# Performance work log

Measured on AMD Instinct MI355X. Metric: run time of the kernel, lower is better.

## Reference

```python
import jax, jax.numpy as jnp
import numpy as np

B, H, D, N = 4, 16, 64, 2048

def setup_inputs() -> dict:
    key = jax.random.key(0)
    kq, kk, kv = jax.random.split(key, 3)
    q = jax.random.normal(kq, (B, H, D, N), dtype=jnp.float32)
    k = jax.random.normal(kk, (B, H, D, N), dtype=jnp.float32)
    v = jax.random.normal(kv, (B, H, D, N), dtype=jnp.float32)
    return {"q": q, "k": k, "v": v}

def reference(q, k, v):
    # layout: (b, h, d, n); scale uses head_dim = q.shape[-2]
    scale = q.shape[-2] ** (-0.5)
    sim = jnp.einsum('bhdi,bhdj->bhij', q * scale, k)  # [B,H,N,N]
    attn = jax.nn.softmax(sim, axis=-1)  # stable softmax (internally subtracts max)
    out = jnp.einsum('bhij,bhdj->bhdi', attn, v)  # [B,H,D,N]
    return out
```

## Files before the change

### kernel.cpp

```cpp
#include <hip/hip_runtime.h>


#define DDIM 64
#define NSEQ 2048
#define STR  72
#define ROWB (STR * 2)
#define BUFB (128 * ROWB)

typedef _Float16 half8   __attribute__((ext_vector_type(8)));
typedef _Float16 half4v  __attribute__((ext_vector_type(4)));
typedef _Float16 half2v  __attribute__((ext_vector_type(2)));
typedef float    float4v __attribute__((ext_vector_type(4)));

__global__ __launch_bounds__(256, 2) void attn_fwd(
    const float* __restrict__ qg, const float* __restrict__ kg,
    const float* __restrict__ vg, float* __restrict__ og) {
  __shared__ __align__(16) char smem[2 * BUFB];

  const int t    = threadIdx.x;
  const int lane = t & 63;
  const int w    = t >> 6;
  const int n16  = lane & 15;
  const int quad = lane >> 4;

  const int bid  = blockIdx.x;
  const int head = ((bid & 7) << 3) | (bid >> 6);
  const int tile = (bid >> 3) & 7;
  const int i0   = tile * 256;

  const float* qh = qg + (size_t)head * DDIM * NSEQ;
  const float* kh = kg + (size_t)head * DDIM * NSEQ;
  const float* vh = vg + (size_t)head * DDIM * NSEQ;

  const int dp  = t & 31;
  const int iqq = t >> 5;
  const int vd  = t >> 2;
  const int qq  = t & 3;

  const float* kp = kh + (2 * dp) * NSEQ;
  const float* vp = vh + vd * NSEQ;

  float4v ka0, kb0, ka1, kb1, va0, vb0, va1, vb1;
  ka0 = *(const float4v*)(kp + iqq * 4);
  kb0 = *(const float4v*)(kp + NSEQ + iqq * 4);
  ka1 = *(const float4v*)(kp + (iqq + 8) * 4);
  kb1 = *(const float4v*)(kp + NSEQ + (iqq + 8) * 4);
  va0 = *(const float4v*)(vp + qq * 4);
  vb0 = *(const float4v*)(vp + qq * 4 + 16);
  va1 = *(const float4v*)(vp + 32 + qq * 4);
  vb1 = *(const float4v*)(vp + 48 + qq * 4);

  {
    _Float16* Qt = (_Float16*)smem;
    const float mul = 0.125f * 1.44269504088896340736f;
#pragma unroll
    for (int h = 0; h < 8; ++h) {
      const float* r0 = qh + (2 * dp) * NSEQ + i0 + h * 32 + iqq * 4;
      float4v a = *(const float4v*)(r0);
      float4v b = *(const float4v*)(r0 + NSEQ);
      _Float16* base = Qt + (h * 32 + iqq * 4) * STR + 2 * dp;
#pragma unroll
      for (int s = 0; s < 4; ++s) {
        half2v hh = {(_Float16)(a[s] * mul), (_Float16)(b[s] * mul)};
        *(half2v*)(base + s * STR) = hh;
      }
    }
  }
  __syncthreads();

  const _Float16* Qt = (const _Float16*)smem;
  half8 bq[4][2];
#pragma unroll
  for (int ig = 0; ig < 4; ++ig) {
    bq[ig][0] = *(const half8*)(Qt + (w * 64 + ig * 16 + n16) * STR + quad * 8);
    bq[ig][1] = *(const half8*)(Qt + (w * 64 + ig * 16 + n16) * STR + 32 + quad * 8);
  }
  __syncthreads();

  const half8 ones = {1.0f16, 1.0f16, 1.0f16, 1.0f16,
                      1.0f16, 1.0f16, 1.0f16, 1.0f16};

  float4v o[4][4];
  float4v lac[4];
#pragma unroll
  for (int ig = 0; ig < 4; ++ig) {
#pragma unroll
    for (int dt = 0; dt < 4; ++dt) o[ig][dt] = (float4v){0.f, 0.f, 0.f, 0.f};
    lac[ig] = (float4v){0.f, 0.f, 0.f, 0.f};
  }

  {
    _Float16* Ktw = (_Float16*)(smem + BUFB);
    _Float16* baseA = Ktw + (iqq * 4) * STR + 2 * dp;
    _Float16* baseB = Ktw + ((iqq + 8) * 4) * STR + 2 * dp;
#pragma unroll
    for (int s = 0; s < 4; ++s) {
      half2v ha = {(_Float16)ka0[s], (_Float16)kb0[s]};
      *(half2v*)(baseA + s * STR) = ha;
      half2v hb = {(_Float16)ka1[s], (_Float16)kb1[s]};
      *(half2v*)(baseB + s * STR) = hb;
    }
    _Float16* Vw = Ktw + 64 * STR + vd * STR;
    half8 h0 = {(_Float16)va0[0], (_Float16)va0[1], (_Float16)va0[2], (_Float16)va0[3],
                (_Float16)vb0[0], (_Float16)vb0[1], (_Float16)vb0[2], (_Float16)vb0[3]};
    *(half8*)(Vw + qq * 8) = h0;
    half8 h1 = {(_Float16)va1[0], (_Float16)va1[1], (_Float16)va1[2], (_Float16)va1[3],
                (_Float16)vb1[0], (_Float16)vb1[1], (_Float16)vb1[2], (_Float16)vb1[3]};
    *(half8*)(Vw + (qq + 4) * 8) = h1;
  }
  __syncthreads();

  for (int kt = 0; kt < 32; ++kt) {
    const _Float16* Kt = (const _Float16*)(smem + ((kt + 1) & 1) * BUFB);
    const _Float16* Vt = Kt + 64 * STR;

    if (kt < 31) {
      const int j1 = (kt + 1) * 64;
      ka0 = *(const float4v*)(kp + j1 + iqq * 4);
      kb0 = *(const float4v*)(kp + NSEQ + j1 + iqq * 4);
      ka1 = *(const float4v*)(kp + j1 + (iqq + 8) * 4);
      kb1 = *(const float4v*)(kp + NSEQ + j1 + (iqq + 8) * 4);
      va0 = *(const float4v*)(vp + j1 + qq * 4);
      vb0 = *(const float4v*)(vp + j1 + qq * 4 + 16);
      va1 = *(const float4v*)(vp + j1 + 32 + qq * 4);
      vb1 = *(const float4v*)(vp + j1 + 48 + qq * 4);
    }

    half4v p[4][4];
#pragma unroll
    for (int jt = 0; jt < 4; ++jt) {
      half8 kfa = *(const half8*)(Kt + (jt * 16 + n16) * STR + quad * 8);
      half8 kfb = *(const half8*)(Kt + (jt * 16 + n16) * STR + 32 + quad * 8);
#pragma unroll
      for (int ig = 0; ig < 4; ++ig) {
        float4v sa = {0.f, 0.f, 0.f, 0.f};
        sa = __builtin_amdgcn_mfma_f32_16x16x32_f16(kfa, bq[ig][0], sa, 0, 0, 0);
        sa = __builtin_amdgcn_mfma_f32_16x16x32_f16(kfb, bq[ig][1], sa, 0, 0, 0);
        p[ig][jt] = (half4v){(_Float16)__builtin_amdgcn_exp2f(sa[0]),
                             (_Float16)__builtin_amdgcn_exp2f(sa[1]),
                             (_Float16)__builtin_amdgcn_exp2f(sa[2]),
                             (_Float16)__builtin_amdgcn_exp2f(sa[3])};
      }
    }

    half8 pg[4][2];
#pragma unroll
    for (int ig = 0; ig < 4; ++ig) {
      pg[ig][0] = __builtin_shufflevector(p[ig][0], p[ig][1], 0, 1, 2, 3, 4, 5, 6, 7);
      pg[ig][1] = __builtin_shufflevector(p[ig][2], p[ig][3], 0, 1, 2, 3, 4, 5, 6, 7);
    }

#pragma unroll
    for (int ig = 0; ig < 4; ++ig) {
      lac[ig] = __builtin_amdgcn_mfma_f32_16x16x32_f16(ones, pg[ig][0], lac[ig], 0, 0, 0);
      lac[ig] = __builtin_amdgcn_mfma_f32_16x16x32_f16(ones, pg[ig][1], lac[ig], 0, 0, 0);
    }

#pragma unroll
    for (int dt = 0; dt < 4; ++dt) {
#pragma unroll
      for (int g = 0; g < 2; ++g) {
        half8 va = *(const half8*)(Vt + (dt * 16 + n16) * STR + (g * 4 + quad) * 8);
#pragma unroll
        for (int ig = 0; ig < 4; ++ig) {
          o[ig][dt] = __builtin_amdgcn_mfma_f32_16x16x32_f16(
              va, pg[ig][g], o[ig][dt], 0, 0, 0);
        }
      }
    }

    if (kt < 31) {
      _Float16* Ktw = (_Float16*)(smem + (kt & 1) * BUFB);
      _Float16* baseA = Ktw + (iqq * 4) * STR + 2 * dp;
      _Float16* baseB = Ktw + ((iqq + 8) * 4) * STR + 2 * dp;
#pragma unroll
      for (int s = 0; s < 4; ++s) {
        half2v ha = {(_Float16)ka0[s], (_Float16)kb0[s]};
        *(half2v*)(baseA + s * STR) = ha;
        half2v hb = {(_Float16)ka1[s], (_Float16)kb1[s]};
        *(half2v*)(baseB + s * STR) = hb;
      }
      _Float16* Vw = Ktw + 64 * STR + vd * STR;
      half8 h0 = {(_Float16)va0[0], (_Float16)va0[1], (_Float16)va0[2], (_Float16)va0[3],
                  (_Float16)vb0[0], (_Float16)vb0[1], (_Float16)vb0[2], (_Float16)vb0[3]};
      *(half8*)(Vw + qq * 8) = h0;
      half8 h1 = {(_Float16)va1[0], (_Float16)va1[1], (_Float16)va1[2], (_Float16)va1[3],
                  (_Float16)vb1[0], (_Float16)vb1[1], (_Float16)vb1[2], (_Float16)vb1[3]};
      *(half8*)(Vw + (qq + 4) * 8) = h1;
      __syncthreads();
    }
  }

#pragma unroll
  for (int ig = 0; ig < 4; ++ig) {
    const float inv = 1.0f / lac[ig][0];
    float* ob = og + (size_t)head * DDIM * NSEQ + i0 + w * 64 + ig * 16 + n16;
#pragma unroll
    for (int dt = 0; dt < 4; ++dt) {
#pragma unroll
      for (int r = 0; r < 4; ++r) {
        ob[(size_t)(dt * 16 + quad * 4 + r) * NSEQ] = o[ig][dt][r] * inv;
      }
    }
  }
}

extern "C" void kernel_launch(void* const* d_in, const int* in_sizes, int n_in,
                              void* d_out, int out_size, void* d_ws, size_t ws_size,
                              hipStream_t stream) {
  (void)in_sizes; (void)n_in; (void)d_ws; (void)ws_size; (void)out_size;
  const float* q = (const float*)d_in[0];
  const float* k = (const float*)d_in[1];
  const float* v = (const float*)d_in[2];
  attn_fwd<<<dim3(512), dim3(256), 0, stream>>>(q, k, v, (float*)d_out);
}
```

Baseline: 187.1 us.

## Use 512-thread blocks with 32 query rows per wave and MFMA priority boost

Doubles the block to 8 waves, each handling 32 query rows instead of 64, so every K/V tile staged in shared memory is consumed by more waves. The global loads and fp16 staging of K/V are redistributed over twice as many threads, which halves per-thread load registers and accumulators. It also wraps the PV and row-sum MFMA section in s_setprio so waves issuing matrix work get priority over waves loading. The trade-off is less register-level reuse of each K/V fragment per wave, more LDS fragment reads per MFMA, and heavier barrier cost across 8 waves.

```diff
diff --git a/kernel.cpp b/kernel.cpp
--- a/kernel.cpp
+++ b/kernel.cpp
@@ -12,7 +12,7 @@
 typedef _Float16 half2v  __attribute__((ext_vector_type(2)));
 typedef float    float4v __attribute__((ext_vector_type(4)));
 
-__global__ __launch_bounds__(256, 2) void attn_fwd(
+__global__ __launch_bounds__(512, 4) void attn_fwd(
     const float* __restrict__ qg, const float* __restrict__ kg,
     const float* __restrict__ vg, float* __restrict__ og) {
   __shared__ __align__(16) char smem[2 * BUFB];
@@ -32,33 +32,31 @@
   const float* kh = kg + (size_t)head * DDIM * NSEQ;
   const float* vh = vg + (size_t)head * DDIM * NSEQ;
 
-  const int dp  = t & 31;
-  const int iqq = t >> 5;
-  const int vd  = t >> 2;
-  const int qq  = t & 3;
+  const int dp = t & 31;
+  const int iq = t >> 5;
+  const int vd = t >> 3;
+  const int sj = t & 7;
+  const int vg_ = sj >> 2;
+  const int vq  = sj & 3;
 
-  const float* kp = kh + (2 * dp) * NSEQ;
-  const float* vp = vh + vd * NSEQ;
+  const float* kp  = kh + (2 * dp) * NSEQ + iq * 4;
+  const float* vpA = vh + vd * NSEQ + vg_ * 32 + vq * 4;
 
-  float4v ka0, kb0, ka1, kb1, va0, vb0, va1, vb1;
-  ka0 = *(const float4v*)(kp + iqq * 4);
-  kb0 = *(const float4v*)(kp + NSEQ + iqq * 4);
-  ka1 = *(const float4v*)(kp + (iqq + 8) * 4);
-  kb1 = *(const float4v*)(kp + NSEQ + (iqq + 8) * 4);
-  va0 = *(const float4v*)(vp + qq * 4);
-  vb0 = *(const float4v*)(vp + qq * 4 + 16);
-  va1 = *(const float4v*)(vp + 32 + qq * 4);
-  vb1 = *(const float4v*)(vp + 48 + qq * 4);
+  float4v ka, kb, va, vb;
+  ka = *(const float4v*)(kp);
+  kb = *(const float4v*)(kp + NSEQ);
+  va = *(const float4v*)(vpA);
+  vb = *(const float4v*)(vpA + 16);
 
   {
     _Float16* Qt = (_Float16*)smem;
     const float mul = 0.125f * 1.44269504088896340736f;
 #pragma unroll
-    for (int h = 0; h < 8; ++h) {
-      const float* r0 = qh + (2 * dp) * NSEQ + i0 + h * 32 + iqq * 4;
+    for (int h = 0; h < 4; ++h) {
+      const float* r0 = qh + (2 * dp) * NSEQ + i0 + h * 64 + iq * 4;
       float4v a = *(const float4v*)(r0);
       float4v b = *(const float4v*)(r0 + NSEQ);
-      _Float16* base = Qt + (h * 32 + iqq * 4) * STR + 2 * dp;
+      _Float16* base = Qt + (h * 64 + iq * 4) * STR + 2 * dp;
 #pragma unroll
       for (int s = 0; s < 4; ++s) {
         half2v hh = {(_Float16)(a[s] * mul), (_Float16)(b[s] * mul)};
@@ -69,21 +67,21 @@
   __syncthreads();
 
   const _Float16* Qt = (const _Float16*)smem;
-  half8 bq[4][2];
+  half8 bq[2][2];
 #pragma unroll
-  for (int ig = 0; ig < 4; ++ig) {
-    bq[ig][0] = *(const half8*)(Qt + (w * 64 + ig * 16 + n16) * STR + quad * 8);
-    bq[ig][1] = *(const half8*)(Qt + (w * 64 + ig * 16 + n16) * STR + 32 + quad * 8);
+  for (int ig = 0; ig < 2; ++ig) {
+    bq[ig][0] = *(const half8*)(Qt + (w * 32 + ig * 16 + n16) * STR + quad * 8);
+    bq[ig][1] = *(const half8*)(Qt + (w * 32 + ig * 16 + n16) * STR + 32 + quad * 8);
   }
   __syncthreads();
 
   const half8 ones = {1.0f16, 1.0f16, 1.0f16, 1.0f16,
                       1.0f16, 1.0f16, 1.0f16, 1.0f16};
 
-  float4v o[4][4];
-  float4v lac[4];
+  float4v o[2][4];
+  float4v lac[2];
 #pragma unroll
-  for (int ig = 0; ig < 4; ++ig) {
+  for (int ig = 0; ig < 2; ++ig) {
 #pragma unroll
     for (int dt = 0; dt < 4; ++dt) o[ig][dt] = (float4v){0.f, 0.f, 0.f, 0.f};
     lac[ig] = (float4v){0.f, 0.f, 0.f, 0.f};
@@ -91,22 +89,15 @@
 
   {
     _Float16* Ktw = (_Float16*)(smem + BUFB);
-    _Float16* baseA = Ktw + (iqq * 4) * STR + 2 * dp;
-    _Float16* baseB = Ktw + ((iqq + 8) * 4) * STR + 2 * dp;
+    _Float16* base = Ktw + (iq * 4) * STR + 2 * dp;
 #pragma unroll
     for (int s = 0; s < 4; ++s) {
-      half2v ha = {(_Float16)ka0[s], (_Float16)kb0[s]};
-      *(half2v*)(baseA + s * STR) = ha;
-      half2v hb = {(_Float16)ka1[s], (_Float16)kb1[s]};
-      *(half2v*)(baseB + s * STR) = hb;
+      half2v hh = {(_Float16)ka[s], (_Float16)kb[s]};
+      *(half2v*)(base + s * STR) = hh;
     }
-    _Float16* Vw = Ktw + 64 * STR + vd * STR;
-    half8 h0 = {(_Float16)va0[0], (_Float16)va0[1], (_Float16)va0[2], (_Float16)va0[3],
-                (_Float16)vb0[0], (_Float16)vb0[1], (_Float16)vb0[2], (_Float16)vb0[3]};
-    *(half8*)(Vw + qq * 8) = h0;
-    half8 h1 = {(_Float16)va1[0], (_Float16)va1[1], (_Float16)va1[2], (_Float16)va1[3],
-                (_Float16)vb1[0], (_Float16)vb1[1], (_Float16)vb1[2], (_Float16)vb1[3]};
-    *(half8*)(Vw + (qq + 4) * 8) = h1;
+    half8 hv = {(_Float16)va[0], (_Float16)va[1], (_Float16)va[2], (_Float16)va[3],
+                (_Float16)vb[0], (_Float16)vb[1], (_Float16)vb[2], (_Float16)vb[3]};
+    *(half8*)(Ktw + 64 * STR + vd * STR + sj * 8) = hv;
   }
   __syncthreads();
 
@@ -116,23 +107,19 @@
 
     if (kt < 31) {
       const int j1 = (kt + 1) * 64;
-      ka0 = *(const float4v*)(kp + j1 + iqq * 4);
-      kb0 = *(const float4v*)(kp + NSEQ + j1 + iqq * 4);
-      ka1 = *(const float4v*)(kp + j1 + (iqq + 8) * 4);
-      kb1 = *(const float4v*)(kp + NSEQ + j1 + (iqq + 8) * 4);
-      va0 = *(const float4v*)(vp + j1 + qq * 4);
-      vb0 = *(const float4v*)(vp + j1 + qq * 4 + 16);
-      va1 = *(const float4v*)(vp + j1 + 32 + qq * 4);
-      vb1 = *(const float4v*)(vp + j1 + 48 + qq * 4);
+      ka = *(const float4v*)(kp + j1);
+      kb = *(const float4v*)(kp + NSEQ + j1);
+      va = *(const float4v*)(vpA + j1);
+      vb = *(const float4v*)(vpA + j1 + 16);
     }
 
-    half4v p[4][4];
+    half4v p[2][4];
 #pragma unroll
     for (int jt = 0; jt < 4; ++jt) {
       half8 kfa = *(const half8*)(Kt + (jt * 16 + n16) * STR + quad * 8);
       half8 kfb = *(const half8*)(Kt + (jt * 16 + n16) * STR + 32 + quad * 8);
 #pragma unroll
-      for (int ig = 0; ig < 4; ++ig) {
+      for (int ig = 0; ig < 2; ++ig) {
         float4v sa = {0.f, 0.f, 0.f, 0.f};
         sa = __builtin_amdgcn_mfma_f32_16x16x32_f16(kfa, bq[ig][0], sa, 0, 0, 0);
         sa = __builtin_amdgcn_mfma_f32_16x16x32_f16(kfb, bq[ig][1], sa, 0, 0, 0);
@@ -143,58 +130,52 @@
       }
     }
 
-    half8 pg[4][2];
+    half8 pg[2][2];
 #pragma unroll
-    for (int ig = 0; ig < 4; ++ig) {
+    for (int ig = 0; ig < 2; ++ig) {
       pg[ig][0] = __builtin_shufflevector(p[ig][0], p[ig][1], 0, 1, 2, 3, 4, 5, 6, 7);
       pg[ig][1] = __builtin_shufflevector(p[ig][2], p[ig][3], 0, 1, 2, 3, 4, 5, 6, 7);
     }
 
+    __builtin_amdgcn_s_setprio(1);
 #pragma unroll
-    for (int ig = 0; ig < 4; ++ig) {
+    for (int ig = 0; ig < 2; ++ig) {
       lac[ig] = __builtin_amdgcn_mfma_f32_16x16x32_f16(ones, pg[ig][0], lac[ig], 0, 0, 0);
       lac[ig] = __builtin_amdgcn_mfma_f32_16x16x32_f16(ones, pg[ig][1], lac[ig], 0, 0, 0);
     }
-
 #pragma unroll
     for (int dt = 0; dt < 4; ++dt) {
 #pragma unroll
       for (int g = 0; g < 2; ++g) {
-        half8 va = *(const half8*)(Vt + (dt * 16 + n16) * STR + (g * 4 + quad) * 8);
+        half8 vaf = *(const half8*)(Vt + (dt * 16 + n16) * STR + (g * 4 + quad) * 8);
 #pragma unroll
-        for (int ig = 0; ig < 4; ++ig) {
+        for (int ig = 0; ig < 2; ++ig) {
           o[ig][dt] = __builtin_amdgcn_mfma_f32_16x16x32_f16(
-              va, pg[ig][g], o[ig][dt], 0, 0, 0);
+              vaf, pg[ig][g], o[ig][dt], 0, 0, 0);
         }
       }
     }
+    __builtin_amdgcn_s_setprio(0);
 
     if (kt < 31) {
       _Float16* Ktw = (_Float16*)(smem + (kt & 1) * BUFB);
-      _Float16* baseA = Ktw + (iqq * 4) * STR + 2 * dp;
-      _Float16* baseB = Ktw + ((iqq + 8) * 4) * STR + 2 * dp;
+      _Float16* base = Ktw + (iq * 4) * STR + 2 * dp;
 #pragma unroll
       for (int s = 0; s < 4; ++s) {
-        half2v ha = {(_Float16)ka0[s], (_Float16)kb0[s]};
-        *(half2v*)(baseA + s * STR) = ha;
-        half2v hb = {(_Float16)ka1[s], (_Float16)kb1[s]};
-        *(half2v*)(baseB + s * STR) = hb;
+        half2v hh = {(_Float16)ka[s], (_Float16)kb[s]};
+        *(half2v*)(base + s * STR) = hh;
       }
-      _Float16* Vw = Ktw + 64 * STR + vd * STR;
-      half8 h0 = {(_Float16)va0[0], (_Float16)va0[1], (_Float16)va0[2], (_Float16)va0[3],
-                  (_Float16)vb0[0], (_Float16)vb0[1], (_Float16)vb0[2], (_Float16)vb0[3]};
-      *(half8*)(Vw + qq * 8) = h0;
-      half8 h1 = {(_Float16)va1[0], (_Float16)va1[1], (_Float16)va1[2], (_Float16)va1[3],
-                  (_Float16)vb1[0], (_Float16)vb1[1], (_Float16)vb1[2], (_Float16)vb1[3]};
-      *(half8*)(Vw + (qq + 4) * 8) = h1;
+      half8 hv = {(_Float16)va[0], (_Float16)va[1], (_Float16)va[2], (_Float16)va[3],
+                  (_Float16)vb[0], (_Float16)vb[1], (_Float16)vb[2], (_Float16)vb[3]};
+      *(half8*)(Ktw + 64 * STR + vd * STR + sj * 8) = hv;
       __syncthreads();
     }
   }
 
 #pragma unroll
-  for (int ig = 0; ig < 4; ++ig) {
+  for (int ig = 0; ig < 2; ++ig) {
     const float inv = 1.0f / lac[ig][0];
-    float* ob = og + (size_t)head * DDIM * NSEQ + i0 + w * 64 + ig * 16 + n16;
+    float* ob = og + (size_t)head * DDIM * NSEQ + i0 + w * 32 + ig * 16 + n16;
 #pragma unroll
     for (int dt = 0; dt < 4; ++dt) {
 #pragma unroll
@@ -212,5 +193,5 @@
   const float* q = (const float*)d_in[0];
   const float* k = (const float*)d_in[1];
   const float* v = (const float*)d_in[2];
-  attn_fwd<<<dim3(512), dim3(256), 0, stream>>>(q, k, v, (float*)d_out);
+  attn_fwd<<<dim3(512), dim3(512), 0, stream>>>(q, k, v, (float*)d_out);
 }
```

Result: no change. 184.3 us (-1.5%).
